# Performance work log

Measured on AMD Instinct MI355X. Metric: run time of the kernel, lower is better.

Reference implementation:

```python
import jax, jax.numpy as jnp
import numpy as np

T, B, IN, H, E = 100, 1, 36, 256, 2048


def setup_inputs() -> dict:
    key = jax.random.key(0)
    ks = jax.random.split(key, 18)
    rn = lambda k, shape, s=1.0: jax.random.normal(k, shape, jnp.float32) * s
    return dict(
        Y=rn(ks[0], (T, B, IN)),
        h0=rn(ks[1], (1, B, H)),
        c0=rn(ks[2], (1, B, H)),
        outEncoder=rn(ks[3], (E, H), 0.1),
        W_ih=rn(ks[4], (4 * H, IN), 0.1),
        W_hh=rn(ks[5], (4 * H, H), 0.1),
        b_ih=rn(ks[6], (4 * H,), 0.1),
        b_hh=rn(ks[7], (4 * H,), 0.1),
        att_W=rn(ks[8], (H, H), 0.1),
        att_V=rn(ks[9], (H, H), 0.1),
        att_b=rn(ks[10], (H, 1), 0.1),
        att_vector=rn(ks[11], (1, H), 0.1),
        W1=rn(ks[12], (H, 2 * H), 0.1),
        b1=rn(ks[13], (H,), 0.1),
        W2=rn(ks[14], (H, H), 0.1),
        b2=rn(ks[15], (H,), 0.1),
        W3=rn(ks[16], (IN, H), 0.1),
        b3=rn(ks[17], (IN,), 0.1),
    )


def reference(Y, h0, c0, outEncoder, W_ih, W_hh, b_ih, b_hh,
              att_W, att_V, att_b, att_vector, W1, b1, W2, b2, W3, b3):
    h = jnp.squeeze(h0, 0)  # [B,H]
    c = jnp.squeeze(c0, 0)  # [B,H]
    # VOut = att_V @ outEncoder^T is timestep-invariant: precompute. [H,E]
    VOut = att_V @ outEncoder.T

    def step(carry, y):
        h, c = carry  # h: [B,H], c: [B,H] (context from prev step after step 0)
        gates = y @ W_ih.T + b_ih + h @ W_hh.T + b_hh  # [B,4H]
        i_g, f_g, g_g, o_g = jnp.split(gates, 4, axis=1)
        cLSTM = jax.nn.sigmoid(f_g) * c + jax.nn.sigmoid(i_g) * jnp.tanh(g_g)
        h_new = jax.nn.sigmoid(o_g) * jnp.tanh(cLSTM)  # [B,H]
        # additive attention: hidden expanded to every encoder position
        WS = att_W @ h_new.T  # [H,1], broadcasts over E columns
        Escore = jnp.tanh(WS + VOut + att_b)  # [H,E]
        scores = att_vector @ Escore  # [1,E]
        alpha = jax.nn.softmax(scores, axis=-1)  # [1,E]
        ctx = alpha @ outEncoder  # [1,H]
        # MLP on concat(new cell state, context)
        v = jnp.concatenate([cLSTM, ctx], axis=1)  # [1,2H]
        v = jax.nn.relu(v @ W1.T + b1)
        v = jax.nn.relu(v @ W2.T + b2)
        out = v @ W3.T + b3  # [1,36]
        # NB: original feeds the attention context back as the LSTM cell state
        return (h_new, ctx), out

    (_, c_final), outputs = jax.lax.scan(step, (h, c), Y)
    return outputs, c_final  # outputs: [100,1,36]
```

## Files before the change

kernel.cpp:

```cpp
#include <hip/hip_runtime.h>
#include <stdint.h>


static constexpr float    L2E = 1.44269504088896341f;
static constexpr float    K2  = 2.88539008177792681f;
static constexpr unsigned SPIN_LIMIT = 200000u;
static constexpr int      FSTRIDE = 16;

static constexpr size_t OFF_BC   = 0;
static constexpr size_t OFF_YG   = 524288;
static constexpr size_t OFF_GRAW = 626688;
static constexpr size_t OFF_CRAW = 729088;
static constexpr size_t CRAW_CP  = 25600;
static constexpr size_t OFF_STOT = 831488;
static constexpr size_t OFF_V1   = 857216;
static constexpr size_t OFF_V2   = 882816;
static constexpr size_t OFF_SYNC = 908416;

__device__ __forceinline__ float exp2fast(float x){ return __builtin_amdgcn_exp2f(x); }
__device__ __forceinline__ float rcpfast(float x){ return __builtin_amdgcn_rcpf(x); }
__device__ __forceinline__ float sigf(float x){ return rcpfast(1.f + exp2fast(-x*L2E)); }
__device__ __forceinline__ float tanhfast(float x){
  float E = exp2fast(x*K2);
  return 1.f - 2.f*rcpfast(E + 1.f);
}
__device__ __forceinline__ unsigned short f2bf(float f){
  unsigned b = __float_as_uint(f);
  return (unsigned short)((b + 0x7FFFu + ((b>>16)&1u))>>16);
}
__device__ __forceinline__ float bf2f(unsigned short u){ return __uint_as_float(((unsigned)u)<<16); }

__device__ __forceinline__ void gstore(float* p, float v){
  __hip_atomic_store(p, v, __ATOMIC_RELAXED, __HIP_MEMORY_SCOPE_AGENT);
}
__device__ __forceinline__ float gload(const float* p){
  return __hip_atomic_load(p, __ATOMIC_RELAXED, __HIP_MEMORY_SCOPE_AGENT);
}
__device__ __forceinline__ void gstore_u32(unsigned* p, unsigned v){
  __hip_atomic_store(p, v, __ATOMIC_RELAXED, __HIP_MEMORY_SCOPE_AGENT);
}
__device__ __forceinline__ unsigned gload_u32(const unsigned* p){
  return __hip_atomic_load(p, __ATOMIC_RELAXED, __HIP_MEMORY_SCOPE_AGENT);
}
__device__ __forceinline__ void gatomic_addf(float* p, float v){
  (void)__hip_atomic_fetch_add(p, v, __ATOMIC_RELAXED, __HIP_MEMORY_SCOPE_AGENT);
}

__device__ __forceinline__ void fbar(unsigned* flags, int w, unsigned ep){
  asm volatile("s_waitcnt vmcnt(0)" ::: "memory");
  __syncthreads();
  if (threadIdx.x == 0) gstore_u32(&flags[w*FSTRIDE], ep);
  if (threadIdx.x < 64) {
    int lane = threadIdx.x;
    unsigned it = 0;
    for (;;) {
      unsigned v = (lane < 32) ? gload_u32(&flags[lane*FSTRIDE]) : ep;
      if (__all((int)(v >= ep))) break;
      __builtin_amdgcn_s_sleep(1);
      if (++it > SPIN_LIMIT) break;
    }
  }
  __syncthreads();
}
__device__ __forceinline__ void fwait_sleep(unsigned* flags, unsigned ep){
  if (threadIdx.x < 64) {
    int lane = threadIdx.x;
    unsigned it = 0;
    for (;;) {
      unsigned v = (lane < 32) ? gload_u32(&flags[lane*FSTRIDE]) : ep;
      if (__all((int)(v >= ep))) break;
      __builtin_amdgcn_s_sleep(2);
      if (++it > SPIN_LIMIT) break;
    }
  }
  __syncthreads();
}
__device__ __forceinline__ void arrive_cnt(unsigned* cnt){
  asm volatile("s_waitcnt vmcnt(0)" ::: "memory");
  __syncthreads();
  if (threadIdx.x == 0)
    __hip_atomic_fetch_add(cnt, 1u, __ATOMIC_RELAXED, __HIP_MEMORY_SCOPE_AGENT);
}
__device__ __forceinline__ void poll_ge(unsigned* p, unsigned tgt){
  if (threadIdx.x == 0){
    unsigned it = 0;
    while (gload_u32(p) < tgt){
      __builtin_amdgcn_s_sleep(2);
      if (++it > SPIN_LIMIT) break;
    }
  }
  __syncthreads();
}

__global__ __launch_bounds__(256) void rnn_prep(
    const float* __restrict__ Y, const float* __restrict__ h0,
    const float* __restrict__ outE, const float* __restrict__ W_ih,
    const float* __restrict__ W_hh, const float* __restrict__ b_ih,
    const float* __restrict__ b_hh, const float* __restrict__ att_V,
    const float* __restrict__ att_b, float* __restrict__ ws)
{
  __shared__ float avT[32*257];
  __shared__ float oeL[8*257];
  __shared__ float yL[40];
  __shared__ float h0L[256];
  const int b = blockIdx.x, tid = threadIdx.x;
  float* ws_bc   = ws + OFF_BC;
  float* ws_yg   = ws + OFF_YG;
  float* ws_graw = ws + OFF_GRAW;

  if (b < 256) {
    int e0 = b*8;
    for (int r=0;r<8;r++) oeL[r*257 + tid] = outE[(size_t)(e0+r)*256 + tid];
    int hl = tid & 31, er = tid >> 5;
    for (int ht=0; ht<8; ++ht) {
      __syncthreads();
      for (int i=0;i<32;i++){ int lin = tid + i*256; int r = lin>>8, j = lin&255;
        avT[r*257 + j] = att_V[(size_t)(ht*32+r)*256 + j]; }
      __syncthreads();
      float acc = 0.f;
      for (int j=0;j<256;j++) acc = fmaf(avT[hl*257 + j], oeL[er*257 + j], acc);
      int h = ht*32 + hl;
      ws_bc[(size_t)(e0+er)*256 + h] = (acc + att_b[h]) * K2;
    }
  } else if (b < 260) {
    int g = b - 256;
    for (int u=0; u<25; ++u) {
      int t = g*25 + u;
      __syncthreads();
      if (tid < 36) yL[tid] = Y[t*36 + tid];
      __syncthreads();
      for (int q=0;q<4;q++){
        int i = tid + 256*q;
        float acc = b_ih[i] + b_hh[i];
        for (int j=0;j<36;j++) acc = fmaf(W_ih[(size_t)i*36 + j], yL[j], acc);
        ws_yg[(size_t)t*1024 + i] = acc;
      }
    }
  } else if (b < 292) {
    int s = b - 260;
    if (tid < 256) h0L[tid] = h0[tid];
    if (tid < 36)  yL[tid]  = Y[tid];
    __syncthreads();
    int r = tid>>3, l8 = tid&7;
    int R = s*32 + r;
    float acc = 0.f;
    for (int q=0;q<32;q++){ int j = l8*32 + q; acc = fmaf(W_hh[(size_t)R*256 + j], h0L[j], acc); }
    acc += __shfl_xor(acc,1); acc += __shfl_xor(acc,2); acc += __shfl_xor(acc,4);
    if (l8 == 0){
      float full = acc + b_ih[R] + b_hh[R];
      for (int j=0;j<36;j++) full = fmaf(W_ih[(size_t)R*36 + j], yL[j], full);
      ws_graw[R] = full;
    }
  } else if (b == 292) {
    unsigned* s0 = (unsigned*)(ws + OFF_SYNC);
    #pragma unroll
    for (int k=0;k<4;k++) gstore_u32(&s0[tid + k*256], 0u);
  } else if (b == 293) {
    if (tid < 128) gstore(&ws[OFF_STOT + tid], 0.f);
  } else {
    int t = b - 294;
    #pragma unroll
    for (int c=0;c<4;c++)
      gstore(&ws[OFF_CRAW + (size_t)c*CRAW_CP + (size_t)t*256 + tid], 0.f);
  }
}

__global__ __launch_bounds__(512, 2) void rnn_main(
    const float* __restrict__ c0, const float* __restrict__ outE,
    const float* __restrict__ W_hh, const float* __restrict__ att_W,
    const float* __restrict__ att_vec,
    const float* __restrict__ W1, const float* __restrict__ b1,
    const float* __restrict__ W2, const float* __restrict__ b2,
    const float* __restrict__ W3, const float* __restrict__ b3,
    float* __restrict__ out, float* __restrict__ ws)
{
  __shared__ __align__(16) unsigned char smem[140288];
  const int w = blockIdx.x;
  const int tid = threadIdx.x;

  float* ws_yg    = ws + OFF_YG;
  float* ws_graw  = ws + OFF_GRAW;
  float* ws_craw  = ws + OFF_CRAW;
  float* ws_stot  = ws + OFF_STOT;
  float* ws_v1    = ws + OFF_V1;
  float* ws_v2    = ws + OFF_V2;
  unsigned* flags = (unsigned*)(ws + OFF_SYNC);
  unsigned* fv1   = flags + 512;
  unsigned* fv2   = flags + 768;

  if (w < 32) {
    float*          bcS    = (float*)(smem);
    unsigned short* oeS    = (unsigned short*)(smem + 67584);
    float*          whhS   = (float*)(smem + 100352);
    float*          wsS    = (float*)(smem + 133632);
    float*          hS     = (float*)(smem + 134688);
    float*          scoreS = (float*)(smem + 135712);
    float*          avS    = (float*)(smem + 138272);

    unsigned awP[64];
    { int r = tid>>1, p = tid&1;
      const float* arow = att_W + (size_t)r*256 + p*128;
      #pragma unroll
      for (int q=0;q<64;q++){
        unsigned lo = f2bf(arow[2*q]);
        unsigned hi = f2bf(arow[2*q+1]);
        awP[q] = lo | (hi<<16);
      } }
    float Vpart = 0.f;
    { int l8 = tid & 7;
      #pragma unroll
      for (int k=0;k<32;k++) Vpart += att_vec[l8*32 + k]; }

    const float* ws_bc = ws + OFF_BC;
    for (int i=0;i<32;i++){ int lin = tid + i*512; int col = lin>>8, h = lin&255;
      bcS[col*264 + h + (h>>5)] = ws_bc[(size_t)(w*64+col)*256 + h]; }
    for (int i=0;i<32;i++){ int lin = tid + i*512; int col = lin>>8, h = lin&255;
      oeS[col*256 + h] = f2bf(outE[(size_t)(w*64+col)*256 + h]); }
    for (int i=0;i<16;i++){ int lin = tid + i*512; int r = lin>>8, j = lin&255;
      whhS[r*260 + j] = W_hh[(size_t)(w*32+r)*256 + j]; }
    if (tid < 256) avS[tid + (tid>>5)] = -2.f * att_vec[tid];
    __syncthreads();

    for (int t = 0; t < 100; ++t) {
      float ig, fg, gg, og;
      float cr0, cr1, cr2, cr3, st;
      float ygn = 0.f;
      int   gr32 = (tid - 256) >> 3, gl8 = tid & 7;
      if (tid < 256) {
        const float* g = ws_graw + (size_t)t*1024;
        ig = gload(&g[tid]);     fg = gload(&g[256+tid]);
        gg = gload(&g[512+tid]); og = gload(&g[768+tid]);
        if (t > 0) {
          const float* cb = ws_craw + (size_t)(t-1)*256 + tid;
          cr0 = gload(cb);             cr1 = gload(cb + CRAW_CP);
          cr2 = gload(cb + 2*CRAW_CP); cr3 = gload(cb + 3*CRAW_CP);
          st  = gload(&ws_stot[t-1]);
        }
      } else if (t <= 98 && gl8 == 0) {
        ygn = ws_yg[(size_t)(t+1)*1024 + w*32 + gr32];
      }
      if (tid < 256) {
        float c;
        if (t == 0) c = c0[tid];
        else        c = ((cr0+cr1)+(cr2+cr3)) * rcpfast(st);
        float cl = sigf(fg)*c + sigf(ig)*tanhfast(gg);
        float hn = sigf(og)*tanhfast(cl);
        hS[tid] = hn;
      }
      __syncthreads();
      { int r = tid>>1, p = tid&1;
        const float4* h4 = (const float4*)(hS + p*128);
        float acc = 0.f;
        #pragma unroll
        for (int i=0;i<32;i++){
          float4 hv = h4[i];
          unsigned pk0 = awP[2*i], pk1 = awP[2*i+1];
          acc = fmaf(__uint_as_float(pk0<<16),           hv.x, acc);
          acc = fmaf(__uint_as_float(pk0 & 0xffff0000u), hv.y, acc);
          acc = fmaf(__uint_as_float(pk1<<16),           hv.z, acc);
          acc = fmaf(__uint_as_float(pk1 & 0xffff0000u), hv.w, acc);
        }
        acc += __shfl_xor(acc, 1);
        if (p == 0) wsS[r + (r>>5)] = acc * K2; }
      __syncthreads();
      { int col = tid >> 3, l8 = tid & 7;
        const float* bcR = bcS + col*264 + l8*33;
        const float* wsR = wsS + l8*33;
        const float* avR = avS + l8*33;
        float acc = Vpart;
        #pragma unroll
        for (int k=0;k<32;k++){
          float E = exp2fast(bcR[k] + wsR[k]);
          acc = fmaf(avR[k], rcpfast(E + 1.f), acc);
        }
        acc += __shfl_xor(acc,1); acc += __shfl_xor(acc,2); acc += __shfl_xor(acc,4);
        if (l8 == 0) scoreS[col] = acc; }
      __syncthreads();
      if (tid < 256) {
        const unsigned short* oeC = oeS + tid;
        float accp = 0.f, sw = 0.f;
        #pragma unroll
        for (int lc=0; lc<64; ++lc){
          float ev = exp2fast(scoreS[lc] * L2E);
          sw += ev;
          accp = fmaf(ev, bf2f(oeC[lc*256]), accp);
        }
        gatomic_addf(&ws_craw[(size_t)(w>>3)*CRAW_CP + (size_t)t*256 + tid], accp);
        if (tid == 0) gatomic_addf(&ws_stot[t], sw);
      } else if (t <= 98) {
        float acc2 = 0.f;
        #pragma unroll
        for (int q=0;q<32;q++){ int j = gl8 + 8*q; acc2 = fmaf(whhS[gr32*260 + j], hS[j], acc2); }
        acc2 += __shfl_xor(acc2,1); acc2 += __shfl_xor(acc2,2); acc2 += __shfl_xor(acc2,4);
        if (gl8 == 0)
          gstore(&ws_graw[(size_t)(t+1)*1024 + w*32 + gr32], acc2 + ygn);
      }
      fbar(flags, w, (unsigned)(t+1));
    }
    if (w == 0 && tid < 256) {
      const float* cb = ws_craw + (size_t)99*256 + tid;
      float rsum = (gload(cb) + gload(cb + CRAW_CP))
                 + (gload(cb + 2*CRAW_CP) + gload(cb + 3*CRAW_CP));
      out[3600 + tid] = rsum * rcpfast(gload(&ws_stot[99]));
    }
  } else if (w < 36) {
    float* wmS = (float*)(smem);
    float* vbS = (float*)(smem + 133632);
    int m = w - 32;
    for (int i=0;i<64;i++){ int lin = tid + i*512; int r = lin>>9, k = lin&511;
      wmS[r*520 + k + (k>>6)] = W1[(size_t)(m*64+r)*512 + k]; }
    __syncthreads();
    for (int s=0; s<100; ++s){
      fwait_sleep(flags, (unsigned)(s+1));
      { float val;
        if (tid < 256) {
          const float* g = ws_graw + (size_t)s*1024;
          float ig = gload(&g[tid]);     float fg = gload(&g[256+tid]);
          float gg = gload(&g[512+tid]);
          float c;
          if (s == 0) c = c0[tid];
          else {
            const float* cb = ws_craw + (size_t)(s-1)*256 + tid;
            float a0 = gload(cb);             float a1 = gload(cb + CRAW_CP);
            float a2 = gload(cb + 2*CRAW_CP); float a3 = gload(cb + 3*CRAW_CP);
            c = ((a0+a1)+(a2+a3)) * rcpfast(gload(&ws_stot[s-1]));
          }
          val = sigf(fg)*c + sigf(ig)*tanhfast(gg);
        } else {
          const float* cb = ws_craw + (size_t)s*256 + (tid-256);
          float rsum = (gload(cb) + gload(cb + CRAW_CP))
                     + (gload(cb + 2*CRAW_CP) + gload(cb + 3*CRAW_CP));
          val = rsum * rcpfast(gload(&ws_stot[s]));
        }
        vbS[tid + (tid>>6)] = val; }
      __syncthreads();
      int row = tid >> 3, l8 = tid & 7;
      const float* wr = wmS + row*520 + l8*65;
      const float* vr = vbS + l8*65;
      float acc = 0.f;
      #pragma unroll
      for (int q=0;q<64;q++) acc = fmaf(wr[q], vr[q], acc);
      acc += __shfl_xor(acc,1); acc += __shfl_xor(acc,2); acc += __shfl_xor(acc,4);
      if (l8 == 0){ int i = m*64 + row; gstore(&ws_v1[(size_t)s*256 + i], fmaxf(acc + b1[i], 0.f)); }
      arrive_cnt(&fv1[s]);
      __syncthreads();
    }
  } else if (w < 38) {
    float* wmS = (float*)(smem);
    float* vbS = (float*)(smem + 133632);
    int m = w - 36;
    for (int i=0;i<64;i++){ int lin = tid + i*512; int r = lin>>8, k = lin&255;
      wmS[r*260 + k + (k>>6)] = W2[(size_t)(m*128+r)*256 + k]; }
    __syncthreads();
    for (int s=0; s<100; ++s){
      poll_ge(&fv1[s], 4u);
      if (tid < 256) vbS[tid + (tid>>6)] = gload(&ws_v1[(size_t)s*256 + tid]);
      __syncthreads();
      int row = tid >> 2, l4 = tid & 3;
      const float* wr = wmS + row*260 + l4*65;
      const float* vr = vbS + l4*65;
      float acc = 0.f;
      #pragma unroll
      for (int q=0;q<64;q++) acc = fmaf(wr[q], vr[q], acc);
      acc += __shfl_xor(acc,1); acc += __shfl_xor(acc,2);
      if (l4 == 0){ int i = m*128 + row; gstore(&ws_v2[(size_t)s*256 + i], fmaxf(acc + b2[i], 0.f)); }
      arrive_cnt(&fv2[s]);
      __syncthreads();
    }
  } else {
    float* wmS = (float*)(smem);
    float* vbS = (float*)(smem + 37440);
    for (int lin = tid; lin < 36*256; lin += 512){ int r = lin>>8, k = lin&255;
      wmS[r*260 + k + (k>>6)] = W3[(size_t)r*256 + k]; }
    __syncthreads();
    for (int s=0; s<100; ++s){
      poll_ge(&fv2[s], 2u);
      if (tid < 256) vbS[tid + (tid>>6)] = gload(&ws_v2[(size_t)s*256 + tid]);
      __syncthreads();
      if (tid < 288) {
        int row = tid >> 3, l8 = tid & 7;
        int kb = l8*32;
        const float* wr = wmS + row*260 + kb + (kb>>6);
        const float* vr = vbS + kb + (kb>>6);
        float acc = 0.f;
        #pragma unroll
        for (int q=0;q<32;q++) acc = fmaf(wr[q], vr[q], acc);
        acc += __shfl_xor(acc,1); acc += __shfl_xor(acc,2); acc += __shfl_xor(acc,4);
        if (l8 == 0) out[s*36 + row] = acc + b3[row];
      }
      __syncthreads();
    }
  }
}

extern "C" void kernel_launch(void* const* d_in, const int* in_sizes, int n_in,
                              void* d_out, int out_size, void* d_ws, size_t ws_size,
                              hipStream_t stream) {
  (void)in_sizes; (void)n_in; (void)out_size; (void)ws_size;
  const float* Y       = (const float*)d_in[0];
  const float* h0      = (const float*)d_in[1];
  const float* c0      = (const float*)d_in[2];
  const float* outEnc  = (const float*)d_in[3];
  const float* W_ih    = (const float*)d_in[4];
  const float* W_hh    = (const float*)d_in[5];
  const float* b_ih    = (const float*)d_in[6];
  const float* b_hh    = (const float*)d_in[7];
  const float* att_W   = (const float*)d_in[8];
  const float* att_V   = (const float*)d_in[9];
  const float* att_b   = (const float*)d_in[10];
  const float* att_vec = (const float*)d_in[11];
  const float* W1      = (const float*)d_in[12];
  const float* b1      = (const float*)d_in[13];
  const float* W2      = (const float*)d_in[14];
  const float* b2      = (const float*)d_in[15];
  const float* W3      = (const float*)d_in[16];
  const float* b3      = (const float*)d_in[17];
  float* out = (float*)d_out;
  float* ws  = (float*)d_ws;

  rnn_prep<<<dim3(394), dim3(256), 0, stream>>>(Y, h0, outEnc, W_ih, W_hh, b_ih, b_hh,
                                                att_V, att_b, ws);
  rnn_main<<<dim3(39), dim3(512), 0, stream>>>(c0, outEnc, W_hh, att_W, att_vec,
                                               W1, b1, W2, b2, W3, b3, out, ws);
}
```

Before: 773.4 us.

## Rebalance score computation onto half the threads and precompute softmax exponentials once

The attention score loop now runs on 256 threads with 4 lanes per column, each doing 64 terms, instead of all 512 threads with 8 lanes per column. This frees the upper 256 threads to compute the W_hh gate products at the same time, rather than in a separate phase. The 64 exponentials and their sum are now computed once by one wavefront into shared memory, instead of every context thread recomputing all 64 exponentials. In exchange the per-thread score work doubles and an extra barrier is added per step.

```diff
diff --git a/kernel.cpp b/kernel.cpp
--- a/kernel.cpp
+++ b/kernel.cpp
@@ -195,6 +195,7 @@
     float*          wsS    = (float*)(smem + 133632);
     float*          hS     = (float*)(smem + 134688);
     float*          scoreS = (float*)(smem + 135712);
+    float*          wexpS  = (float*)(smem + 135968);
     float*          avS    = (float*)(smem + 138272);
 
     unsigned awP[64];
@@ -207,9 +208,9 @@
         awP[q] = lo | (hi<<16);
       } }
     float Vpart = 0.f;
-    { int l8 = tid & 7;
+    { int l4 = tid & 3;
       #pragma unroll
-      for (int k=0;k<32;k++) Vpart += att_vec[l8*32 + k]; }
+      for (int k=0;k<64;k++) Vpart += att_vec[l4*64 + k]; }
 
     const float* ws_bc = ws + OFF_BC;
     for (int i=0;i<32;i++){ int lin = tid + i*512; int col = lin>>8, h = lin&255;
@@ -263,30 +264,24 @@
         acc += __shfl_xor(acc, 1);
         if (p == 0) wsS[r + (r>>5)] = acc * K2; }
       __syncthreads();
-      { int col = tid >> 3, l8 = tid & 7;
-        const float* bcR = bcS + col*264 + l8*33;
-        const float* wsR = wsS + l8*33;
-        const float* avR = avS + l8*33;
+      if (tid < 256) {
+        int col = tid >> 2, l4 = tid & 3;
+        const float* bcR = bcS + col*264 + l4*66;
+        const float* wsR = wsS + l4*66;
+        const float* avR = avS + l4*66;
         float acc = Vpart;
         #pragma unroll
         for (int k=0;k<32;k++){
           float E = exp2fast(bcR[k] + wsR[k]);
           acc = fmaf(avR[k], rcpfast(E + 1.f), acc);
         }
-        acc += __shfl_xor(acc,1); acc += __shfl_xor(acc,2); acc += __shfl_xor(acc,4);
-        if (l8 == 0) scoreS[col] = acc; }
-      __syncthreads();
-      if (tid < 256) {
-        const unsigned short* oeC = oeS + tid;
-        float accp = 0.f, sw = 0.f;
-        #pragma unroll
-        for (int lc=0; lc<64; ++lc){
-          float ev = exp2fast(scoreS[lc] * L2E);
-          sw += ev;
-          accp = fmaf(ev, bf2f(oeC[lc*256]), accp);
+        #pragma unroll
+        for (int k=0;k<32;k++){
+          float E = exp2fast(bcR[33+k] + wsR[33+k]);
+          acc = fmaf(avR[33+k], rcpfast(E + 1.f), acc);
         }
-        gatomic_addf(&ws_craw[(size_t)(w>>3)*CRAW_CP + (size_t)t*256 + tid], accp);
-        if (tid == 0) gatomic_addf(&ws_stot[t], sw);
+        acc += __shfl_xor(acc,1); acc += __shfl_xor(acc,2);
+        if (l4 == 0) scoreS[col] = acc;
       } else if (t <= 98) {
         float acc2 = 0.f;
         #pragma unroll
@@ -294,6 +289,24 @@
         acc2 += __shfl_xor(acc2,1); acc2 += __shfl_xor(acc2,2); acc2 += __shfl_xor(acc2,4);
         if (gl8 == 0)
           gstore(&ws_graw[(size_t)(t+1)*1024 + w*32 + gr32], acc2 + ygn);
+      }
+      __syncthreads();
+      if (tid < 64) {
+        float ev = exp2fast(scoreS[tid] * L2E);
+        wexpS[tid] = ev;
+        float s = ev;
+        #pragma unroll
+        for (int d=1; d<64; d<<=1) s += __shfl_xor(s, d);
+        if (tid == 0) gatomic_addf(&ws_stot[t], s);
+      }
+      __syncthreads();
+      if (tid < 256) {
+        const unsigned short* oeC = oeS + tid;
+        float accp = 0.f;
+        #pragma unroll
+        for (int lc=0; lc<64; ++lc)
+          accp = fmaf(wexpS[lc], bf2f(oeC[lc*256]), accp);
+        gatomic_addf(&ws_craw[(size_t)(w>>3)*CRAW_CP + (size_t)t*256 + tid], accp);
       }
       fbar(flags, w, (unsigned)(t+1));
     }
```

Measured after the change: 645.2 us. 16.6% less time.
